# Performance work log

Measured on AMD Instinct MI355X. Metric: run time of the kernel, lower is better.

The kernel has to match this reference:

```python
import jax, jax.numpy as jnp
import numpy as np

LAMBDA_W = 1.0
NEG_INF = -1e10


def setup_inputs() -> dict:
    key = jax.random.key(0)
    k1, k2, k3 = jax.random.split(key, 3)
    B, L, D = 8, 2048, 256
    h_x = jax.random.normal(k1, (B, L, D), dtype=jnp.float32)
    h_y = jax.random.normal(k2, (B, L, D), dtype=jnp.float32)
    # masks: valid prefix of 3/4 length, padded tail of zeros (exercises masking)
    valid = (3 * L) // 4
    base = (jnp.arange(L) < valid).astype(jnp.float32)
    x_mask = jnp.broadcast_to(base, (B, L))
    y_mask = jnp.broadcast_to(base, (B, L))
    # biaffine weight (n_label=1, no biases), init_value scaling kept at O(1)
    W = jax.random.normal(k3, (D, D), dtype=jnp.float32) / jnp.sqrt(jnp.float32(D))
    return {"h_x": h_x, "h_y": h_y, "x_mask": x_mask, "y_mask": y_mask, "W": W}


def reference(h_x, h_y, x_mask, y_mask, W):
    # src = h_x [B,Ls,D], pred = h_y [B,Lp,D]
    src, pred = h_x, h_y
    src_mask, pred_mask = x_mask, y_mask

    # cost_mx[b,p,s] = ||src[b,s] - pred[b,p]||_2, via ||a||^2+||b||^2-2ab
    src_sq = jnp.sum(src * src, axis=-1)            # [B,Ls]
    pred_sq = jnp.sum(pred * pred, axis=-1)         # [B,Lp]
    cross = jnp.einsum('bpd,bsd->bps', pred, src)   # [B,Lp,Ls]
    cost_mx = jnp.sqrt(jnp.maximum(pred_sq[:, :, None] + src_sq[:, None, :] - 2.0 * cross, 0.0))

    # biaffine scores: pred W src^T  -> [B,Lp,Ls]
    tr_mx = jnp.einsum('bpd,de,bse->bps', pred, W, src)

    # cost_mask[b,p,s] = pred_mask[b,p]*src_mask[b,s]
    cost_mask = pred_mask[:, :, None] * src_mask[:, None, :]
    tr_mx = jnp.where(cost_mask == 0, NEG_INF, tr_mx)
    tr_prob = jax.nn.softmax(tr_mx, axis=-1)

    flow_cost = tr_prob * cost_mx                   # [B,Lp,Ls]

    nL1 = jnp.sum(pred_mask, axis=-1, keepdims=True)  # [B,1]
    nL2 = jnp.sum(src_mask, axis=-1, keepdims=True)   # [B,1]
    fc = jnp.sum(flow_cost, axis=(1, 2), keepdims=True)  # [B,1,1]
    fc = fc / (nL1 * nL2)   # broadcasts [B,1,1]/[B,1] -> [B,B,1], matches torch
    fc = jnp.mean(fc)
    return fc * LAMBDA_W
```

## Files before the change

### kernel.cpp

```cpp
#include <hip/hip_runtime.h>
#include <math.h>
#include <stdint.h>

#define B_ 8
#define L_ 2048
#define D_ 256
#define NEG_INF_V (-1e10f)
#define NSTRIP 32

typedef __bf16 bf16x8 __attribute__((ext_vector_type(8)));
typedef float f32x4 __attribute__((ext_vector_type(4)));

#define MFMA16(a, b, c) __builtin_amdgcn_mfma_f32_16x16x32_bf16((a), (b), (c), 0, 0, 0)


__global__ __launch_bounds__(256) void convert_kernel(
    const float* __restrict__ x, const float* __restrict__ y,
    const float* __restrict__ W,
    __bf16* __restrict__ srcFM, __bf16* __restrict__ predFM,
    __bf16* __restrict__ WFM,
    float* __restrict__ src_sq, float* __restrict__ pred_sq) {
    int tid = threadIdx.x;
    int blk = blockIdx.x;
    if (blk < 2048) {
        const float* in = (blk < 1024) ? x : y;
        __bf16* out = (blk < 1024) ? srcFM : predFM;
        float* sqout = (blk < 1024) ? src_sq : pred_sq;
        int g = blk & 1023;
        __shared__ __align__(16) __bf16 sFM[512 * 8];
        __shared__ float sSQ[16];
        int kb = (tid & 31) >> 2, qq = tid & 3;
        #pragma unroll
        for (int pass = 0; pass < 2; ++pass) {
            int m = pass * 8 + (tid >> 5);
            const float* p = in + ((size_t)g * 16 + m) * D_ + (tid & 31) * 8;
            float4 v0 = *(const float4*)p;
            float4 v1 = *(const float4*)(p + 4);
            float ss = v0.x * v0.x + v0.y * v0.y + v0.z * v0.z + v0.w * v0.w +
                       v1.x * v1.x + v1.y * v1.y + v1.z * v1.z + v1.w * v1.w;
            #pragma unroll
            for (int o = 16; o > 0; o >>= 1) ss += __shfl_xor(ss, o, 64);
            if ((tid & 31) == 0) sSQ[m] = ss;
            union { __bf16 o[8]; bf16x8 v; } cv;
            cv.o[0] = (__bf16)v0.x; cv.o[1] = (__bf16)v0.y;
            cv.o[2] = (__bf16)v0.z; cv.o[3] = (__bf16)v0.w;
            cv.o[4] = (__bf16)v1.x; cv.o[5] = (__bf16)v1.y;
            cv.o[6] = (__bf16)v1.z; cv.o[7] = (__bf16)v1.w;
            *(bf16x8*)(sFM + (m * 32 + kb * 4 + qq) * 8) = cv.v;
        }
        __syncthreads();
        int G0 = tid * 2;
        int kb0 = G0 >> 6, q0 = (G0 >> 4) & 3, m0 = G0 & 15;
        bf16x8 a = *(const bf16x8*)(sFM + (m0 * 32 + kb0 * 4 + q0) * 8);
        bf16x8 bgr = *(const bf16x8*)(sFM + ((m0 + 1) * 32 + kb0 * 4 + q0) * 8);
        *(bf16x8*)(out + ((size_t)g * 512 + G0) * 8) = a;
        *(bf16x8*)(out + ((size_t)g * 512 + G0 + 1) * 8) = bgr;
        if (tid < 16) sqout[g * 16 + tid] = sSQ[tid];
    } else {
        int idx = (blk - 2048) * 256 + tid;
        int m = idx & 15, q = (idx >> 4) & 3, kb = (idx >> 6) & 7, gn = idx >> 9;
        union { __bf16 o[8]; bf16x8 v; } cv;
        #pragma unroll
        for (int j = 0; j < 8; ++j)
            cv.o[j] = (__bf16)W[(size_t)(kb * 32 + q * 8 + j) * D_ + gn * 16 + m];
        *(bf16x8*)(WFM + (size_t)idx * 8) = cv.v;
    }
}

__global__ __launch_bounds__(256, 2) void predw_mfma(
    const __bf16* __restrict__ predFM, const __bf16* __restrict__ WFM,
    const float* __restrict__ pred_mask, __bf16* __restrict__ pwFM) {
    __shared__ __align__(16) __bf16 sT[128 * 136];
    __shared__ int flag;
    int tid = threadIdx.x, lane = tid & 63, wid = tid >> 6;
    int wp = wid >> 1, wn = wid & 1;
    int id = blockIdx.x;
    int m0 = (((id >> 3) & 15) + (id & 7) * 16) * 128;
    int n0 = (id >> 7) * 128;
    if (tid == 0) flag = 0;
    __syncthreads();
    if (tid < 128) { if (pred_mask[m0 + tid] != 0.f) atomicOr(&flag, 1); }
    __syncthreads();
    if (!flag) return;

    const __bf16* bA = predFM + (size_t)(m0 / 16 + wp * 4) * 4096 + lane * 8;
    const __bf16* bB = WFM + (size_t)(n0 / 16 + wn * 4) * 4096 + lane * 8;
    f32x4 acc[4][4] = {};
    #pragma unroll
    for (int kb = 0; kb < 8; ++kb) {
        bf16x8 fA[4], fB[4];
        #pragma unroll
        for (int t = 0; t < 4; ++t) {
            fA[t] = *(const bf16x8*)(bA + (t * 8 + kb) * 512);
            fB[t] = *(const bf16x8*)(bB + (t * 8 + kb) * 512);
        }
        #pragma unroll
        for (int pt = 0; pt < 4; ++pt)
            #pragma unroll
            for (int st = 0; st < 4; ++st)
                acc[pt][st] = MFMA16(fA[pt], fB[st], acc[pt][st]);
    }
    int q = lane >> 4, cn = lane & 15;
    #pragma unroll
    for (int pt = 0; pt < 4; ++pt)
        #pragma unroll
        for (int st = 0; st < 4; ++st)
            #pragma unroll
            for (int r = 0; r < 4; ++r)
                sT[(wp * 64 + pt * 16 + q * 4 + r) * 136 + wn * 64 + st * 16 + cn] =
                    (__bf16)acc[pt][st][r];
    __syncthreads();
    #pragma unroll
    for (int i = 0; i < 8; ++i) {
        int idx = i * 256 + tid;
        int gl = idx >> 8, kbl = (idx >> 6) & 3, qq = (idx >> 4) & 3, mm = idx & 15;
        bf16x8 v = *(const bf16x8*)(sT + (gl * 16 + mm) * 136 + kbl * 32 + qq * 8);
        *(bf16x8*)(pwFM +
                   (((size_t)(m0 / 16 + gl) * 8 + n0 / 32 + kbl) * 64 + qq * 16 + mm) * 8) = v;
    }
}

__global__ __launch_bounds__(256, 3) void fused_mfma(
    const __bf16* __restrict__ srcFM, const __bf16* __restrict__ predFM,
    const __bf16* __restrict__ pwFM,
    const float* __restrict__ src_mask, const float* __restrict__ pred_mask,
    const float* __restrict__ src_sq, const float* __restrict__ pred_sq,
    float* __restrict__ m_part, float* __restrict__ l_part,
    float* __restrict__ w_part, float* __restrict__ Sarr,
    unsigned int* __restrict__ counter) {
    __shared__ __align__(16) __bf16 sS[64 * 256];
    __shared__ float sPM[128], sPSQ[128], sSM[64], sSSQ[64];
    __shared__ int flg[4];
    int tid = threadIdx.x, lane = tid & 63, wid = tid >> 6;
    int id = blockIdx.x;
    int b = id & 7, px = (id >> 3) & 15, syb = id >> 7;
    int p0 = px * 128, s0 = syb * 64;

    if (id == 0) {
        if (tid == 0) *counter = 0u;
        if (tid < 24) Sarr[tid] = 0.f;
    }
    if (tid < 4) flg[tid] = 0;
    __syncthreads();
    if (tid < 128) {
        float v = pred_mask[b * L_ + p0 + tid];
        sPM[tid] = v;
        sPSQ[tid] = pred_sq[b * L_ + p0 + tid];
        atomicOr(&flg[(v != 0.f) ? 0 : 1], 1);
    } else if (tid < 192) {
        int t = tid - 128;
        float v = src_mask[b * L_ + s0 + t];
        sSM[t] = v;
        sSSQ[t] = src_sq[b * L_ + s0 + t];
        atomicOr(&flg[(v != 0.f) ? 2 : 3], 1);
    }
    {
        const __bf16* g = srcFM + ((size_t)(b * 128 + syb * 4)) * 4096;
        #pragma unroll
        for (int i = 0; i < 8; ++i) {
            size_t off = (size_t)i * 2048 + tid * 8;
            *(bf16x8*)(sS + off) = *(const bf16x8*)(g + off);
        }
    }
    __syncthreads();
    const bool anyVP = flg[0] != 0, anyIP = flg[1] != 0, anyVS = flg[2] != 0;
    const bool doT = anyVP && anyVS;
    const bool doG = anyVS || anyIP;
    if (!doG) {
        if (tid < 128) {
            size_t o = (size_t)syb * (B_ * L_) + b * L_ + p0 + tid;
            m_part[o] = NEG_INF_V; l_part[o] = 64.f; w_part[o] = 0.f;
        }
        return;
    }

    const __bf16* bP = predFM + ((size_t)(b * 128 + px * 8 + wid * 2)) * 4096 + lane * 8;
    const __bf16* bW = pwFM + ((size_t)(b * 128 + px * 8 + wid * 2)) * 4096 + lane * 8;
    const __bf16* bS = sS + lane * 8;

    f32x4 aG[2][4] = {};
    f32x4 aT[2][4] = {};
    if (doT) {
        #pragma unroll
        for (int kb = 0; kb < 8; ++kb) {
            bf16x8 fP[2], fW[2], fB[4];
            #pragma unroll
            for (int m = 0; m < 2; ++m) {
                fP[m] = *(const bf16x8*)(bP + (m * 8 + kb) * 512);
                fW[m] = *(const bf16x8*)(bW + (m * 8 + kb) * 512);
            }
            #pragma unroll
            for (int t = 0; t < 4; ++t)
                fB[t] = *(const bf16x8*)(bS + (t * 8 + kb) * 512);
            #pragma unroll
            for (int m = 0; m < 2; ++m)
                #pragma unroll
                for (int t = 0; t < 4; ++t) {
                    aG[m][t] = MFMA16(fP[m], fB[t], aG[m][t]);
                    aT[m][t] = MFMA16(fW[m], fB[t], aT[m][t]);
                }
        }
    } else {
        #pragma unroll
        for (int kb = 0; kb < 8; ++kb) {
            bf16x8 fP[2], fB[4];
            #pragma unroll
            for (int m = 0; m < 2; ++m)
                fP[m] = *(const bf16x8*)(bP + (m * 8 + kb) * 512);
            #pragma unroll
            for (int t = 0; t < 4; ++t)
                fB[t] = *(const bf16x8*)(bS + (t * 8 + kb) * 512);
            #pragma unroll
            for (int m = 0; m < 2; ++m)
                #pragma unroll
                for (int t = 0; t < 4; ++t)
                    aG[m][t] = MFMA16(fP[m], fB[t], aG[m][t]);
        }
    }

    int q = lane >> 4, cn = lane & 15;
    float smv[4], sqv[4];
    #pragma unroll
    for (int t = 0; t < 4; ++t) {
        smv[t] = sSM[t * 16 + cn];
        sqv[t] = sSSQ[t * 16 + cn];
    }
    if (doT) {
        #pragma unroll
        for (int m = 0; m < 2; ++m) {
            int rbase = wid * 32 + m * 16 + q * 4;
            #pragma unroll
            for (int r = 0; r < 4; ++r) {
                float pm = sPM[rbase + r], psq = sPSQ[rbase + r];
                float tv[4], cst[4];
                float tm = -1e30f;
                #pragma unroll
                for (int t = 0; t < 4; ++t) {
                    cst[t] = __builtin_amdgcn_sqrtf(
                        fmaxf(psq + sqv[t] - 2.f * aG[m][t][r], 0.f));
                    float tt = aT[m][t][r];
                    tv[t] = (pm == 0.f) ? 0.f : (smv[t] != 0.f ? tt : NEG_INF_V);
                    tm = fmaxf(tm, tv[t]);
                }
                #pragma unroll
                for (int o = 8; o > 0; o >>= 1) tm = fmaxf(tm, __shfl_xor(tm, o, 16));
                float l = 0.f, w = 0.f;
                #pragma unroll
                for (int t = 0; t < 4; ++t) {
                    float e = __expf(tv[t] - tm);
                    l += e;
                    w = fmaf(e, cst[t], w);
                }
                #pragma unroll
                for (int o = 8; o > 0; o >>= 1) {
                    l += __shfl_xor(l, o, 16);
                    w += __shfl_xor(w, o, 16);
                }
                if (cn == 0) {
                    size_t o = (size_t)syb * (B_ * L_) + b * L_ + p0 + rbase + r;
                    m_part[o] = tm;
                    l_part[o] = l;
                    w_part[o] = w;
                }
            }
        }
    } else {
        #pragma unroll
        for (int m = 0; m < 2; ++m) {
            int rbase = wid * 32 + m * 16 + q * 4;
            #pragma unroll
            for (int r = 0; r < 4; ++r) {
                float pm = sPM[rbase + r], psq = sPSQ[rbase + r];
                float w = 0.f;
                #pragma unroll
                for (int t = 0; t < 4; ++t) {
                    float cst = __builtin_amdgcn_sqrtf(
                        fmaxf(psq + sqv[t] - 2.f * aG[m][t][r], 0.f));
                    w += cst;
                }
                #pragma unroll
                for (int o = 8; o > 0; o >>= 1) w += __shfl_xor(w, o, 16);
                if (cn == 0) {
                    size_t o = (size_t)syb * (B_ * L_) + b * L_ + p0 + rbase + r;
                    m_part[o] = (pm == 0.f) ? 0.f : NEG_INF_V;
                    l_part[o] = 64.f;
                    w_part[o] = w;
                }
            }
        }
    }
}

__global__ __launch_bounds__(256) void combine_kernel(
    const float* __restrict__ m_part, const float* __restrict__ l_part,
    const float* __restrict__ w_part,
    const float* __restrict__ x_mask, const float* __restrict__ y_mask,
    float* __restrict__ Sarr, unsigned int* __restrict__ counter,
    float* __restrict__ out) {
    int tid = threadIdx.x;
    int r = blockIdx.x * 256 + tid;
    int b = r >> 11;
    float mm = -1e30f;
    #pragma unroll
    for (int s = 0; s < NSTRIP; ++s) mm = fmaxf(mm, m_part[(size_t)s * (B_ * L_) + r]);
    float l = 0.f, w = 0.f;
    #pragma unroll
    for (int s = 0; s < NSTRIP; ++s) {
        size_t o = (size_t)s * (B_ * L_) + r;
        float e = __expf(m_part[o] - mm);
        l = fmaf(l_part[o], e, l);
        w = fmaf(w_part[o], e, w);
    }
    float sv = w / l;
    float n1 = y_mask[r], n2 = x_mask[r];
    __shared__ float red[3][256];
    red[0][tid] = sv; red[1][tid] = n1; red[2][tid] = n2;
    __syncthreads();
    for (int o = 128; o > 0; o >>= 1) {
        if (tid < o) {
            red[0][tid] += red[0][tid + o];
            red[1][tid] += red[1][tid + o];
            red[2][tid] += red[2][tid + o];
        }
        __syncthreads();
    }
    __shared__ int isLast;
    if (tid == 0) {
        atomicAdd(&Sarr[b], red[0][0]);
        atomicAdd(&Sarr[8 + b], red[1][0]);
        atomicAdd(&Sarr[16 + b], red[2][0]);
        __threadfence();
        isLast = (atomicAdd(counter, 1u) == 63u) ? 1 : 0;
    }
    __syncthreads();
    if (isLast) {
        __shared__ float fb[24];
        if (tid < 24) fb[tid] = atomicAdd(&Sarr[tid], 0.f);
        __syncthreads();
        if (tid == 0) {
            float ss = 0.f, si = 0.f;
            for (int bb = 0; bb < B_; bb++) {
                ss += fb[bb];
                si += 1.0f / (fb[8 + bb] * fb[16 + bb]);
            }
            out[0] = ss * si / (float)(B_ * B_);
        }
    }
}

extern "C" void kernel_launch(void* const* d_in, const int* in_sizes, int n_in,
                              void* d_out, int out_size, void* d_ws, size_t ws_size,
                              hipStream_t stream) {
    const float* h_x = (const float*)d_in[0];
    const float* h_y = (const float*)d_in[1];
    const float* x_mask = (const float*)d_in[2];
    const float* y_mask = (const float*)d_in[3];
    const float* W = (const float*)d_in[4];

    char* w8 = (char*)d_ws;
    const size_t BLD2 = (size_t)B_ * L_ * D_ * 2;
    __bf16* srcFM = (__bf16*)w8;
    __bf16* predFM = (__bf16*)(w8 + BLD2);
    __bf16* pwFM = (__bf16*)(w8 + 2 * BLD2);
    __bf16* WFM = (__bf16*)(w8 + 3 * BLD2);
    float* src_sq = (float*)(w8 + 3 * BLD2 + (1 << 17));
    float* pred_sq = (float*)(w8 + 3 * BLD2 + (1 << 17) + (1 << 16));
    char* pbase = w8 + 3 * BLD2 + (1 << 17) + (1 << 17);
    const size_t PSZ = (size_t)B_ * L_ * NSTRIP * 4;
    float* m_part = (float*)pbase;
    float* l_part = (float*)(pbase + PSZ);
    float* w_part = (float*)(pbase + 2 * PSZ);
    float* Sarr = (float*)(pbase + 3 * PSZ);
    unsigned int* counter = (unsigned int*)(pbase + 3 * PSZ + 128);

    convert_kernel<<<2080, 256, 0, stream>>>(h_x, h_y, W, srcFM, predFM, WFM,
                                             src_sq, pred_sq);
    predw_mfma<<<256, 256, 0, stream>>>(predFM, WFM, y_mask, pwFM);
    fused_mfma<<<4096, 256, 0, stream>>>(
        srcFM, predFM, pwFM, x_mask, y_mask, src_sq, pred_sq,
        m_part, l_part, w_part, Sarr, counter);
    combine_kernel<<<B_ * L_ / 256, 256, 0, stream>>>(
        m_part, l_part, w_part, x_mask, y_mask, Sarr, counter, (float*)d_out);
}
```

Measured before the change: 134.7 us.

## Parallelize combine kernel across strips with online-softmax merges

```diff
diff --git a/kernel.cpp b/kernel.cpp
--- a/kernel.cpp
+++ b/kernel.cpp
@@ -297,40 +297,69 @@
     const float* __restrict__ x_mask, const float* __restrict__ y_mask,
     float* __restrict__ Sarr, unsigned int* __restrict__ counter,
     float* __restrict__ out) {
-    int tid = threadIdx.x;
-    int r = blockIdx.x * 256 + tid;
+    int tid = threadIdx.x, lane = tid & 63, wid = tid >> 6;
+    int row = lane & 31, h = lane >> 5;
+    int r = blockIdx.x * 32 + row;
     int b = r >> 11;
-    float mm = -1e30f;
-    #pragma unroll
-    for (int s = 0; s < NSTRIP; ++s) mm = fmaxf(mm, m_part[(size_t)s * (B_ * L_) + r]);
+    int sbase = wid * 8 + h * 4;
+
+    float m4[4], l4[4], w4[4];
+    #pragma unroll
+    for (int i = 0; i < 4; ++i) {
+        size_t o = (size_t)(sbase + i) * (B_ * L_) + r;
+        m4[i] = m_part[o];
+        l4[i] = l_part[o];
+        w4[i] = w_part[o];
+    }
+    float mm = fmaxf(fmaxf(m4[0], m4[1]), fmaxf(m4[2], m4[3]));
     float l = 0.f, w = 0.f;
     #pragma unroll
-    for (int s = 0; s < NSTRIP; ++s) {
-        size_t o = (size_t)s * (B_ * L_) + r;
-        float e = __expf(m_part[o] - mm);
-        l = fmaf(l_part[o], e, l);
-        w = fmaf(w_part[o], e, w);
-    }
-    float sv = w / l;
-    float n1 = y_mask[r], n2 = x_mask[r];
-    __shared__ float red[3][256];
-    red[0][tid] = sv; red[1][tid] = n1; red[2][tid] = n2;
-    __syncthreads();
-    for (int o = 128; o > 0; o >>= 1) {
-        if (tid < o) {
-            red[0][tid] += red[0][tid + o];
-            red[1][tid] += red[1][tid + o];
-            red[2][tid] += red[2][tid + o];
-        }
-        __syncthreads();
+    for (int i = 0; i < 4; ++i) {
+        float e = __expf(m4[i] - mm);
+        l = fmaf(l4[i], e, l);
+        w = fmaf(w4[i], e, w);
+    }
+    {
+        float mo = __shfl_xor(mm, 32, 64);
+        float lo = __shfl_xor(l, 32, 64);
+        float wo = __shfl_xor(w, 32, 64);
+        float M = fmaxf(mm, mo);
+        float e1 = __expf(mm - M), e2 = __expf(mo - M);
+        l = l * e1 + lo * e2;
+        w = w * e1 + wo * e2;
+        mm = M;
+    }
+    __shared__ float sm[4][32], sl[4][32], sw[4][32];
+    if (h == 0) { sm[wid][row] = mm; sl[wid][row] = l; sw[wid][row] = w; }
+    __syncthreads();
+    float sv = 0.f, n1 = 0.f, n2 = 0.f;
+    if (tid < 32) {
+        float M = fmaxf(fmaxf(sm[0][row], sm[1][row]),
+                        fmaxf(sm[2][row], sm[3][row]));
+        float L = 0.f, W = 0.f;
+        #pragma unroll
+        for (int wv = 0; wv < 4; ++wv) {
+            float e = __expf(sm[wv][row] - M);
+            L = fmaf(sl[wv][row], e, L);
+            W = fmaf(sw[wv][row], e, W);
+        }
+        sv = W / L;
+        n1 = y_mask[r];
+        n2 = x_mask[r];
+    }
+    #pragma unroll
+    for (int o = 16; o > 0; o >>= 1) {
+        sv += __shfl_xor(sv, o, 64);
+        n1 += __shfl_xor(n1, o, 64);
+        n2 += __shfl_xor(n2, o, 64);
     }
     __shared__ int isLast;
     if (tid == 0) {
-        atomicAdd(&Sarr[b], red[0][0]);
-        atomicAdd(&Sarr[8 + b], red[1][0]);
-        atomicAdd(&Sarr[16 + b], red[2][0]);
+        atomicAdd(&Sarr[b], sv);
+        atomicAdd(&Sarr[8 + b], n1);
+        atomicAdd(&Sarr[16 + b], n2);
         __threadfence();
-        isLast = (atomicAdd(counter, 1u) == 63u) ? 1 : 0;
+        isLast = (atomicAdd(counter, 1u) == 511u) ? 1 : 0;
     }
     __syncthreads();
     if (isLast) {
@@ -379,6 +408,6 @@
     fused_mfma<<<4096, 256, 0, stream>>>(
         srcFM, predFM, pwFM, x_mask, y_mask, src_sq, pred_sq,
         m_part, l_part, w_part, Sarr, counter);
-    combine_kernel<<<B_ * L_ / 256, 256, 0, stream>>>(
+    combine_kernel<<<512, 256, 0, stream>>>(
         m_part, l_part, w_part, x_mask, y_mask, Sarr, counter, (float*)d_out);
 }
```

New measurement: 150.4 us. +11.6%, slower.
